# Kernel optimization log

Hardware: AMD Instinct MI355X
Metric: run time of the kernel (lower is better)

The kernel has to match this reference:

```python
import jax, jax.numpy as jnp
import numpy as np

B_, C_, H_, W_ = 8, 128, 64, 64
OUT_ = 128
D_MODEL = C_ // 4        # 32, per-chunk channels fed to Mamba
D_STATE = 16
D_CONV = 4
D_INNER = 2 * D_MODEL    # expand=2 -> 64
DT_RANK = max(1, -(-D_MODEL // 16))  # ceil(32/16)=2
SE_RED = 2


def _ln(x, g, b):
    m = x.mean(-1, keepdims=True)
    v = jnp.var(x, axis=-1, keepdims=True)
    return (x - m) / jnp.sqrt(v + 1e-5) * g + b


def _mamba(u, in_W, conv_W, conv_b, xproj_W, dt_W, dt_b, A_log, D_p, out_W):
    # u: (B, L, d_model)
    Bsz, L, _ = u.shape
    xz = u @ in_W.T                                   # (B,L,2*d_inner)
    x, z = jnp.split(xz, 2, axis=-1)
    # causal depthwise conv1d along L
    xc = jnp.swapaxes(x, 1, 2)                        # (B,d_inner,L)
    xc = jax.lax.conv_general_dilated(
        xc, conv_W, (1,), [(D_CONV - 1, 0)],
        feature_group_count=D_INNER,
        dimension_numbers=('NCH', 'OIH', 'NCH'))
    x = jax.nn.silu(jnp.swapaxes(xc + conv_b[None, :, None], 1, 2))
    x_dbl = x @ xproj_W.T                             # (B,L,dt_rank+2*d_state)
    dt, Bm, Cm = jnp.split(x_dbl, [DT_RANK, DT_RANK + D_STATE], axis=-1)
    dt = jax.nn.softplus(dt @ dt_W.T + dt_b)          # (B,L,d_inner)
    A = -jnp.exp(A_log)                               # (d_inner,d_state)
    dA = jnp.exp(dt[..., None] * A)                   # (B,L,d_inner,d_state)
    dBu = dt[..., None] * Bm[:, :, None, :] * x[..., None]

    def step(h, inp):
        dA_t, dBu_t, C_t = inp
        h = dA_t * h + dBu_t                          # (B,d_inner,d_state)
        return h, jnp.einsum('bds,bs->bd', h, C_t)

    h0 = jnp.zeros((Bsz, D_INNER, D_STATE), dtype=x.dtype)
    _, ys = jax.lax.scan(step, h0, (jnp.swapaxes(dA, 0, 1), jnp.swapaxes(dBu, 0, 1), jnp.swapaxes(Cm, 0, 1)))
    y = jnp.swapaxes(ys, 0, 1) + x * D_p
    y = y * jax.nn.silu(z)
    return y @ out_W.T


def _branch(xi, skip_scale, se_W1, se_W2, mp):
    M1 = _mamba(xi, *mp)                              # (B,L,c)
    M2 = skip_scale * xi
    # SE: adaptive avg-pool over spatial == mean over tokens; cat over channels
    y = jnp.concatenate([M1, M2], axis=-1).mean(axis=1)   # (B,2c)
    y = jax.nn.sigmoid(jax.nn.relu(y @ se_W1.T) @ se_W2.T)
    g1, g2 = jnp.split(y, 2, axis=-1)
    return g1[:, None, :] * M1 + g2[:, None, :] * M2


def _pvm(x, norm_g, norm_b, proj_W, proj_b, skip_scale, se_W1, se_W2,
         in_W, conv_W, conv_b, xproj_W, dt_W, dt_b, A_log, D_p, out_W):
    B, C, H, W = x.shape
    L = H * W
    xf = jnp.swapaxes(x.reshape(B, C, L), 1, 2)       # (B,L,C)
    xn = _ln(xf, norm_g, norm_b)
    mp = (in_W, conv_W, conv_b, xproj_W, dt_W, dt_b, A_log, D_p, out_W)
    outs = [_branch(c, skip_scale, se_W1, se_W2, mp) for c in jnp.split(xn, 4, axis=2)]
    xm = jnp.concatenate(outs, axis=2)                # (B,L,C)
    xm = _ln(xm, norm_g, norm_b)
    xm = xm @ proj_W.T + proj_b                       # (B,L,out)
    return jnp.swapaxes(xm, 1, 2).reshape(B, proj_W.shape[0], H, W)


def setup_inputs():
    key = jax.random.key(0)
    ks = jax.random.split(key, 10)
    p = {}
    p['x'] = jax.random.normal(ks[0], (B_, C_, H_, W_), jnp.float32)
    p['norm_g'] = jnp.ones((C_,), jnp.float32)
    p['norm_b'] = jnp.zeros((C_,), jnp.float32)
    p['proj_W'] = jax.random.normal(ks[1], (OUT_, C_), jnp.float32) * 0.05
    p['proj_b'] = jnp.zeros((OUT_,), jnp.float32)
    p['skip_scale'] = jnp.ones((1,), jnp.float32)
    p['se_W1'] = jax.random.normal(ks[2], (SE_RED, 2 * D_MODEL), jnp.float32) * 0.1
    p['se_W2'] = jax.random.normal(ks[3], (2 * D_MODEL, SE_RED), jnp.float32) * 0.1
    p['in_W'] = jax.random.normal(ks[4], (2 * D_INNER, D_MODEL), jnp.float32) * 0.1
    p['conv_W'] = jax.random.normal(ks[5], (D_INNER, 1, D_CONV), jnp.float32) * 0.2
    p['conv_b'] = jnp.zeros((D_INNER,), jnp.float32)
    p['xproj_W'] = jax.random.normal(ks[6], (DT_RANK + 2 * D_STATE, D_INNER), jnp.float32) * 0.1
    p['dt_W'] = jax.random.normal(ks[7], (D_INNER, DT_RANK), jnp.float32) * 0.1
    p['dt_b'] = jnp.full((D_INNER,), -4.6, jnp.float32)  # softplus(-4.6) ~ 0.01 init dt
    p['A_log'] = jnp.log(jnp.broadcast_to(jnp.arange(1.0, D_STATE + 1.0, dtype=jnp.float32), (D_INNER, D_STATE)))
    p['D_p'] = jnp.ones((D_INNER,), jnp.float32)
    p['out_W'] = jax.random.normal(ks[8], (D_MODEL, D_INNER), jnp.float32) * 0.1
    return p


def reference(x, norm_g, norm_b, proj_W, proj_b, skip_scale, se_W1, se_W2,
              in_W, conv_W, conv_b, xproj_W, dt_W, dt_b, A_log, D_p, out_W):
    return _pvm(x, norm_g, norm_b, proj_W, proj_b, skip_scale, se_W1, se_W2,
                in_W, conv_W, conv_b, xproj_W, dt_W, dt_b, A_log, D_p, out_W)
```

## Files before the change

### kernel.cpp

```cpp
#include <hip/hip_runtime.h>
#include <math.h>

typedef _Float16 h16;

#define DEV static __device__ __forceinline__

constexpr int B_ = 8, C_ = 128, L_ = 4096, OUT_ = 128;
constexpr int NCH = 4, DM = 32, DS = 16, DI = 64;
constexpr int NI = 32;
constexpr int NSEG = 128;
constexpr int SL = L_ / NSEG;

DEV float sigmoidf_(float x) { return 1.f / (1.f + __expf(-x)); }
DEV float siluf_(float x) { return x * sigmoidf_(x); }
DEV float softplusf_(float x) { return (x > 20.f) ? x : __logf(1.f + __expf(x)); }

template <int CTRL>
DEV float dpp_add_(float x) {
  int v = __builtin_amdgcn_update_dpp(0, __float_as_int(x), CTRL, 0xf, 0xf, false);
  return x + __int_as_float(v);
}

typedef __attribute__((ext_vector_type(8))) _Float16 f16x8;
typedef __attribute__((ext_vector_type(4))) _Float16 f16x4;
typedef __attribute__((ext_vector_type(4))) float f32x4;

DEV void powladder_(float E, float* out) {
  float E2 = E * E;
  float E4 = E2 * E2;
  float E8 = E4 * E4;
  float E3 = E2 * E;
  out[0] = E;       out[1] = E2;      out[2] = E3;      out[3] = E4;
  out[4] = E4 * E;  out[5] = E4 * E2; out[6] = E4 * E3; out[7] = E8;
  out[8] = E8 * E;  out[9] = E8 * E2; out[10] = E8 * E3; out[11] = E8 * E4;
  out[12] = E8 * out[4]; out[13] = E8 * out[5]; out[14] = E8 * out[6];
  out[15] = E8 * E8;
}

DEV void powladder8_(float E, float* out) {
  float E2 = E * E, E3 = E2 * E, E4 = E2 * E2;
  out[0] = E; out[1] = E2; out[2] = E3; out[3] = E4;
  out[4] = E4 * E; out[5] = E4 * E2; out[6] = E4 * E3; out[7] = E4 * E4;
}

__global__ __launch_bounds__(256) void k0_wcvt(const float* __restrict__ in_W,
                                               const float* __restrict__ xproj_W,
                                               h16* __restrict__ WH) {
  int tid = blockIdx.x * 256 + threadIdx.x;
  if (tid < 4096) {
    WH[tid] = (h16)in_W[tid];
  } else {
    int j = tid - 4096;
    int r = j >> 6;
    WH[tid] = (r < 34) ? (h16)xproj_W[j - (r - (r < 34 ? 0 : 0)) * 0 + (r * 64 + (j & 63)) - j + j] : (h16)0.f;
    WH[tid] = (r < 34) ? (h16)xproj_W[r * 64 + (j & 63)] : (h16)0.f;
  }
}

__global__ __launch_bounds__(256) void k1_ln(const float* __restrict__ x,
                                             const float* __restrict__ gn,
                                             const float* __restrict__ bn,
                                             float* __restrict__ XN,
                                             h16* __restrict__ XNH,
                                             float* __restrict__ SUMXN) {
  int bid = blockIdx.x;
  int b = bid >> 6, tile = bid & 63;
  int t0 = tile * 64;
  int tid = threadIdx.x;
  __shared__ float xT[128][65];
  __shared__ float gnS[128], bnS[128];
  __shared__ float red[256];
  if (tid < 128) { gnS[tid] = gn[tid]; bnS[tid] = bn[tid]; }
  for (int k = tid; k < 8192; k += 256) {
    int c = k >> 6, tt = k & 63;
    xT[c][tt] = x[((size_t)(b * C_ + c)) * L_ + t0 + tt];
  }
  __syncthreads();
  {
    int tok = tid >> 2, q = tid & 3;
    float s = 0.f, qq = 0.f;
#pragma unroll
    for (int j = 0; j < 32; ++j) {
      float v = xT[q + 4 * j][tok];
      s += v; qq += v * v;
    }
    s = dpp_add_<0xB1>(s); qq = dpp_add_<0xB1>(qq);
    s = dpp_add_<0x4E>(s); qq = dpp_add_<0x4E>(qq);
    float m = s * (1.f / 128.f);
    float var = qq * (1.f / 128.f) - m * m;
    float rs = rsqrtf(var + 1e-5f);
#pragma unroll
    for (int j = 0; j < 32; ++j) {
      int c = q + 4 * j;
      float v = xT[c][tok];
      xT[c][tok] = (v - m) * rs * gnS[c] + bnS[c];
    }
  }
  __syncthreads();
  float acc = 0.f;
  int cfix = tid & 127;
  for (int k = tid; k < 8192; k += 256) {
    int tt = k >> 7, c = k & 127;
    float v = xT[c][tt];
    XN[((size_t)(b * L_ + t0 + tt)) * C_ + c] = v;
    acc += v;
  }
  for (int k = tid; k < 1024; k += 256) {
    int tt = k >> 4, c8 = (k & 15) * 8;
    f16x8 hv;
#pragma unroll
    for (int j = 0; j < 8; ++j) hv[j] = (_Float16)xT[c8 + j][tt];
    *(f16x8*)&XNH[((size_t)(b * L_ + t0 + tt)) * C_ + c8] = hv;
  }
  red[tid] = acc;
  __syncthreads();
  if (tid < 128) atomicAdd(&SUMXN[b * C_ + cfix], red[tid] + red[tid + 128]);
}

__global__ __launch_bounds__(256) void k2_prep(
    const h16* __restrict__ WH, const float* __restrict__ conv_W,
    const float* __restrict__ conv_b, const float* __restrict__ dt_W,
    const float* __restrict__ dt_b, const float* __restrict__ A_log,
    const h16* __restrict__ XNH, h16* __restrict__ SX2, h16* __restrict__ SDT2,
    h16* __restrict__ SB2, h16* __restrict__ SC2, h16* __restrict__ SZ2,
    float* __restrict__ Pp, float* __restrict__ Qp) {
  int bid = blockIdx.x;
  int i = bid >> 6, tile = bid & 63;
  int b = i >> 2, ch = i & 3;
  int t0 = tile * 64;
  int tid = threadIdx.x;
  int w = __builtin_amdgcn_readfirstlane(tid >> 6);
  int lane = tid & 63;

  __shared__ __attribute__((aligned(16))) union {
    struct {
      _Float16 uH[80][40];
      _Float16 w1H[64][40];
    } s;
    float xdS[64][36];
    _Float16 zL[64][88];
  } U;
  __shared__ __attribute__((aligned(16))) _Float16 wzH[64][40];
  __shared__ __attribute__((aligned(16))) _Float16 preH[80][66];
  __shared__ __attribute__((aligned(16))) _Float16 xH[64][72];
  __shared__ __attribute__((aligned(16))) _Float16 w2H[48][72];
  __shared__ float convWS[64][4];
  __shared__ float dtWS[64][2];
  __shared__ float dtbS[64], cbS[64];

  convWS[tid >> 2][tid & 3] = conv_W[tid];
  if (tid < 128) dtWS[tid >> 1][tid & 1] = dt_W[tid];
  if (tid < 64) { dtbS[tid] = dt_b[tid]; cbS[tid] = conv_b[tid]; }
  const h16* xnh = XNH + (size_t)b * L_ * C_ + ch * DM;
  for (int k = tid; k < 320; k += 256) {
    int r = k >> 2, c8 = (k & 3) * 8;
    int tg = t0 - 3 + r;
    f16x8 v = {0, 0, 0, 0, 0, 0, 0, 0};
    if (r < 67 && tg >= 0) v = *(const f16x8*)&xnh[(size_t)tg * C_ + c8];
    *(f16x8*)&U.s.uH[r][c8] = v;
  }
  if (tid < 256) {
    int r = tid >> 2, c8 = (tid & 3) * 8;
    *(f16x8*)&U.s.w1H[r][c8] = *(const f16x8*)&WH[r * 32 + c8];
    *(f16x8*)&wzH[r][c8] = *(const f16x8*)&WH[(64 + r) * 32 + c8];
  }
  for (int k = tid; k < 384; k += 256) {
    int r = k >> 3, c8 = (k & 7) * 8;
    *(f16x8*)&w2H[r][c8] = *(const f16x8*)&WH[4096 + r * 64 + c8];
  }
  __syncthreads();

  int rsel = lane & 15, ksel = (lane >> 4) * 8;
  {
    int nt = w;
    f16x8 bf = *(const f16x8*)&U.s.w1H[nt * 16 + rsel][ksel];
    int row0q = (lane >> 4) << 2;
    int col = nt * 16 + rsel;
#pragma unroll
    for (int mt = 0; mt < 5; ++mt) {
      f16x8 af = *(const f16x8*)&U.s.uH[mt * 16 + rsel][ksel];
      f32x4 acc = {0.f, 0.f, 0.f, 0.f};
      acc = __builtin_amdgcn_mfma_f32_16x16x32_f16(af, bf, acc, 0, 0, 0);
      int row0 = mt * 16 + row0q;
#pragma unroll
      for (int r = 0; r < 4; ++r) preH[row0 + r][col] = (_Float16)acc[r];
    }
  }
  f32x4 zacc[4];
  {
    f16x8 bf = *(const f16x8*)&U.s.uH[3 + w * 16 + rsel][ksel];
#pragma unroll
    for (int mt = 0; mt < 4; ++mt) {
      f16x8 af = *(const f16x8*)&wzH[mt * 16 + rsel][ksel];
      f32x4 acc = {0.f, 0.f, 0.f, 0.f};
      zacc[mt] = __builtin_amdgcn_mfma_f32_16x16x32_f16(af, bf, acc, 0, 0, 0);
    }
  }
  __syncthreads();

  h16* SXp = SX2 + ((size_t)i * L_ + t0) * DI;
  for (int k = tid; k < 4096; k += 256) {
    int r = k >> 6, d = k & 63;
    float v = cbS[d];
#pragma unroll
    for (int j = 0; j < 4; ++j) v = fmaf(convWS[d][j], (float)preH[r + j][d], v);
    v = siluf_(v);
    xH[r][d] = (_Float16)v;
    SXp[(size_t)r * DI + d] = (h16)v;
  }
  __syncthreads();

  {
    int mt = w;
    f16x8 a0 = *(const f16x8*)&xH[mt * 16 + rsel][ksel];
    f16x8 a1 = *(const f16x8*)&xH[mt * 16 + rsel][32 + ksel];
    int row0 = mt * 16 + ((lane >> 4) << 2);
#pragma unroll
    for (int nt = 0; nt < 3; ++nt) {
      f16x8 b0 = *(const f16x8*)&w2H[nt * 16 + rsel][ksel];
      f16x8 b1 = *(const f16x8*)&w2H[nt * 16 + rsel][32 + ksel];
      f32x4 acc = {0.f, 0.f, 0.f, 0.f};
      acc = __builtin_amdgcn_mfma_f32_16x16x32_f16(a0, b0, acc, 0, 0, 0);
      acc = __builtin_amdgcn_mfma_f32_16x16x32_f16(a1, b1, acc, 0, 0, 0);
      int col = nt * 16 + rsel;
      if (col < 34) {
#pragma unroll
        for (int r = 0; r < 4; ++r) U.xdS[row0 + r][col] = acc[r];
      }
    }
  }
  __syncthreads();

  h16* dtL = (h16*)&preH[0][0];
  h16* SDTp = SDT2 + ((size_t)i * L_ + t0) * DI;
  for (int k = tid; k < 4096; k += 256) {
    int d = k & 63, r = k >> 6;
    float raw = fmaf(U.xdS[r][0], dtWS[d][0], fmaf(U.xdS[r][1], dtWS[d][1], dtbS[d]));
    float dtv = softplusf_(raw);
    dtL[r * 66 + d] = (_Float16)dtv;
    SDTp[(size_t)r * DI + d] = (h16)dtv;
  }
  h16* SBp = SB2 + ((size_t)i * L_ + t0) * DS;
  h16* SCp = SC2 + ((size_t)i * L_ + t0) * DS;
  for (int k = tid; k < 1024; k += 256) {
    int s = k & 15, r = k >> 4;
    SBp[(size_t)r * DS + s] = (h16)U.xdS[r][2 + s];
    SCp[(size_t)r * DS + s] = (h16)U.xdS[r][18 + s];
  }
  __syncthreads();

  {
    int seg = w >> 1, shalf = w & 1;
    int s0 = shalf * 8;
    float Av[16];
#pragma unroll
    for (int s = 0; s < 16; ++s) Av[s] = -__expf(A_log[lane * 16 + s]);
    float A0 = Av[0];
    bool okf = true;
#pragma unroll
    for (int s = 0; s < 16; ++s)
      okf &= fabsf(Av[s] - (float)(s + 1) * A0) <= 1e-4f * fabsf(Av[s]);
    int fastp = __all(okf ? 1 : 0);
    float h[8];
#pragma unroll
    for (int j = 0; j < 8; ++j) h[j] = 0.f;
    float sdt = 0.f;
    int rowbase = seg * SL;
    for (int t = 0; t < SL; ++t) {
      int row = rowbase + t;
      float dt = (float)dtL[row * 66 + lane];
      float xv = (float)xH[row][lane];
      float dtx = dt * xv;
      float dA[8];
      if (fastp) {
        powladder8_(__expf(A0 * dt), dA);
        if (shalf) {
          float E8 = dA[7];
#pragma unroll
          for (int j = 0; j < 8; ++j) dA[j] *= E8;
        }
      } else {
#pragma unroll
        for (int j = 0; j < 8; ++j) dA[j] = __expf(Av[s0 + j] * dt);
      }
      const float* brow = &U.xdS[row][2 + s0];
#pragma unroll
      for (int j = 0; j < 8; ++j) h[j] = fmaf(dA[j], h[j], dtx * brow[j]);
      sdt += dt;
    }
    float P[8];
    if (fastp) {
      powladder8_(__expf(A0 * sdt), P);
      if (shalf) {
        float E8 = P[7];
#pragma unroll
        for (int j = 0; j < 8; ++j) P[j] *= E8;
      }
    } else {
#pragma unroll
      for (int j = 0; j < 8; ++j) P[j] = __expf(Av[s0 + j] * sdt);
    }
    int segg = tile * 2 + seg;
    size_t base = (((size_t)i * DI + lane) * NSEG + segg) * DS + s0;
    *(float4*)(Pp + base) = *(float4*)&P[0];
    *(float4*)(Pp + base + 4) = *(float4*)&P[4];
    *(float4*)(Qp + base) = *(float4*)&h[0];
    *(float4*)(Qp + base + 4) = *(float4*)&h[4];
  }
  __syncthreads();

  {
    int tok = w * 16 + rsel;
    int zq = (lane >> 4) << 2;
#pragma unroll
    for (int mt = 0; mt < 4; ++mt) {
      f16x4 pk;
#pragma unroll
      for (int r = 0; r < 4; ++r) pk[r] = (_Float16)siluf_(zacc[mt][r]);
      *(f16x4*)&U.zL[tok][mt * 16 + zq] = pk;
    }
  }
  __syncthreads();
  h16* SZp = SZ2 + ((size_t)i * L_ + t0) * DI;
  for (int k = tid; k < 512; k += 256) {
    int r = k >> 3, dblk = (k & 7) * 8;
    f16x8 v = *(const f16x8*)&U.zL[r][dblk];
    *(f16x8*)&SZp[(size_t)r * DI + dblk] = v;
  }
}

__global__ __launch_bounds__(256) void k3b_comb(float* __restrict__ Pp,
                                                const float* __restrict__ Qp) {
  int g = blockIdx.x * 256 + threadIdx.x;
  int s = g & 15;
  int r = g >> 4;
  size_t base = (size_t)r * NSEG * DS + s;
  float H = 0.f;
  for (int seg = 0; seg < NSEG; ++seg) {
    size_t a = base + (size_t)seg * DS;
    float P = Pp[a], Q = Qp[a];
    Pp[a] = H;
    H = fmaf(P, H, Q);
  }
}

__global__ __launch_bounds__(256) void k3c_scan(
    const float* __restrict__ A_log, const h16* __restrict__ SDT2,
    const h16* __restrict__ SX2, const h16* __restrict__ SB2,
    const h16* __restrict__ SC2, const h16* __restrict__ SZ2,
    const float* __restrict__ D_p, const float* __restrict__ H0p,
    h16* __restrict__ YS2, float* __restrict__ SUMYF) {
  int bid = blockIdx.x;
  int i = bid >> 5, sg = bid & 31;
  int tid = threadIdx.x;
  int w = tid >> 6, lane = tid & 63;
  int seg = sg * 4 + w;
  int t0 = seg * SL;
  __shared__ float rowS[4][SL][36];
  {
    int tk = lane & 31, hf = lane >> 5;
    const h16* p = (hf ? SC2 : SB2) + ((size_t)i * L_ + t0 + tk) * DS;
    float4 r0 = *(const float4*)p;
    float4 r1 = *(const float4*)(p + 8);
    const h16* hp0 = (const h16*)&r0;
    const h16* hp1 = (const h16*)&r1;
#pragma unroll
    for (int s = 0; s < 8; ++s) {
      rowS[w][tk][hf * 16 + s] = (float)hp0[s];
      rowS[w][tk][hf * 16 + 8 + s] = (float)hp1[s];
    }
  }
  __syncthreads();
  float Av[16];
#pragma unroll
  for (int s = 0; s < 16; ++s) Av[s] = -__expf(A_log[lane * 16 + s]);
  float A0 = Av[0];
  bool okf = true;
#pragma unroll
  for (int s = 0; s < 16; ++s) okf &= fabsf(Av[s] - (float)(s + 1) * A0) <= 1e-4f * fabsf(Av[s]);
  int fastp = __all(okf ? 1 : 0);
  float Dp = D_p[lane];
  float h[16];
  {
    size_t base = (((size_t)i * DI + lane) * NSEG + seg) * DS;
#pragma unroll
    for (int j = 0; j < 4; ++j) *(float4*)&h[4 * j] = *(const float4*)(H0p + base + 4 * j);
  }
  const h16* pdt = SDT2 + ((size_t)i * L_ + t0) * DI + lane;
  const h16* pxx = SX2 + ((size_t)i * L_ + t0) * DI + lane;
  const h16* pzz = SZ2 + ((size_t)i * L_ + t0) * DI + lane;
  h16* pys = YS2 + ((size_t)i * L_ + t0) * DI + lane;
  float dtc = (float)pdt[0], xvc = (float)pxx[0], zvc = (float)pzz[0];
  float sum = 0.f;
  for (int t = 0; t < SL; ++t) {
    float dt = dtc, xv = xvc, zv = zvc;
    if (t < SL - 1) {
      dtc = (float)pdt[(t + 1) * DI];
      xvc = (float)pxx[(t + 1) * DI];
      zvc = (float)pzz[(t + 1) * DI];
    }
    const float* row = &rowS[w][t][0];
    float Bv[16], Cv[16];
#pragma unroll
    for (int j = 0; j < 4; ++j) {
      *(float4*)&Bv[4 * j] = *(const float4*)(row + 4 * j);
      *(float4*)&Cv[4 * j] = *(const float4*)(row + 16 + 4 * j);
    }
    float dtx = dt * xv;
    float dA[16];
    if (fastp) {
      powladder_(__expf(A0 * dt), dA);
    } else {
#pragma unroll
      for (int s = 0; s < 16; ++s) dA[s] = __expf(Av[s] * dt);
    }
    float y0 = 0.f, y1 = 0.f, y2 = 0.f, y3 = 0.f;
#pragma unroll
    for (int s = 0; s < 16; s += 4) {
      h[s] = fmaf(dA[s], h[s], dtx * Bv[s]);       y0 = fmaf(h[s], Cv[s], y0);
      h[s + 1] = fmaf(dA[s + 1], h[s + 1], dtx * Bv[s + 1]); y1 = fmaf(h[s + 1], Cv[s + 1], y1);
      h[s + 2] = fmaf(dA[s + 2], h[s + 2], dtx * Bv[s + 2]); y2 = fmaf(h[s + 2], Cv[s + 2], y2);
      h[s + 3] = fmaf(dA[s + 3], h[s + 3], dtx * Bv[s + 3]); y3 = fmaf(h[s + 3], Cv[s + 3], y3);
    }
    float y = (y0 + y1) + (y2 + y3);
    float yf = fmaf(xv, Dp, y) * zv;
    pys[(size_t)t * DI] = (h16)yf;
    sum += yf;
  }
  atomicAdd(&SUMYF[i * DI + lane], sum);
}

__global__ __launch_bounds__(64) void k4_gates(
    const float* __restrict__ out_W, const float* __restrict__ se_W1,
    const float* __restrict__ se_W2, const float* __restrict__ skip_p,
    const float* __restrict__ SUMYF, const float* __restrict__ SUMXN,
    float* __restrict__ GATES) {
  int i = blockIdx.x;
  int b = i >> 2, ch = i & 3;
  int tid = threadIdx.x;
  __shared__ float syS[64], catS[64], seS[2];
  syS[tid] = SUMYF[i * DI + tid];
  __syncthreads();
  float invL = 1.f / (float)L_;
  if (tid < 32) {
    float acc = 0.f;
#pragma unroll
    for (int dd = 0; dd < 64; ++dd) acc = fmaf(syS[dd], out_W[tid * 64 + dd], acc);
    catS[tid] = acc * invL;
  } else {
    int c = tid - 32;
    catS[tid] = skip_p[0] * SUMXN[b * C_ + ch * DM + c] * invL;
  }
  __syncthreads();
  if (tid < 2) {
    float acc = 0.f;
#pragma unroll
    for (int k = 0; k < 64; ++k) acc = fmaf(catS[k], se_W1[tid * 64 + k], acc);
    seS[tid] = fmaxf(acc, 0.f);
  }
  __syncthreads();
  float gg = fmaf(seS[0], se_W2[tid * 2 + 0], seS[1] * se_W2[tid * 2 + 1]);
  GATES[i * DI + tid] = sigmoidf_(gg);
}

__global__ __launch_bounds__(256) void k5b_combine(
    const float* __restrict__ out_W, const float* __restrict__ skip_p,
    const float* __restrict__ GATES, const h16* __restrict__ YS2,
    float* __restrict__ XN) {
  int bid = blockIdx.x;
  int i = bid >> 6, tile = bid & 63;
  int b = i >> 2, ch = i & 3;
  int t0 = tile * 64;
  int tid = threadIdx.x;
  int w = __builtin_amdgcn_readfirstlane(tid >> 6);
  int lane = tid & 63;
  __shared__ __attribute__((aligned(16))) _Float16 yH[64][72];
  __shared__ __attribute__((aligned(16))) _Float16 owH[32][72];
  __shared__ float xnS[64][37];
  __shared__ float gS[64];
  if (tid < 64) gS[tid] = GATES[i * DI + tid];
  const h16* py = YS2 + ((size_t)i * L_ + t0) * DI;
  for (int k = tid; k < 512; k += 256) {
    int tt = k >> 3, dblk = (k & 7) * 8;
    *(f16x8*)&yH[tt][dblk] = *(const f16x8*)&py[(size_t)tt * DI + dblk];
  }
  for (int k = tid; k < 2048; k += 256) owH[k >> 6][k & 63] = (_Float16)out_W[k];
  float* xn = XN + (size_t)b * L_ * C_ + ch * DM;
  for (int k = tid; k < 2048; k += 256) {
    int tt = k >> 5, o = k & 31;
    xnS[tt][o] = xn[(size_t)(t0 + tt) * C_ + o];
  }
  __syncthreads();
  int rsel = lane & 15, ksel = (lane >> 4) * 8;
  float skip = skip_p[0];
  int mt = w;
  f16x8 a0 = *(const f16x8*)&yH[mt * 16 + rsel][ksel];
  f16x8 a1 = *(const f16x8*)&yH[mt * 16 + rsel][32 + ksel];
  int row0 = mt * 16 + ((lane >> 4) << 2);
#pragma unroll
  for (int nt = 0; nt < 2; ++nt) {
    f16x8 b0 = *(const f16x8*)&owH[nt * 16 + rsel][ksel];
    f16x8 b1 = *(const f16x8*)&owH[nt * 16 + rsel][32 + ksel];
    f32x4 acc = {0.f, 0.f, 0.f, 0.f};
    acc = __builtin_amdgcn_mfma_f32_16x16x32_f16(a0, b0, acc, 0, 0, 0);
    acc = __builtin_amdgcn_mfma_f32_16x16x32_f16(a1, b1, acc, 0, 0, 0);
    int o = nt * 16 + rsel;
    float g1 = gS[o], g2s = gS[32 + o] * skip;
#pragma unroll
    for (int r = 0; r < 4; ++r) {
      int tok = row0 + r;
      xnS[tok][o] = g1 * acc[r] + g2s * xnS[tok][o];
    }
  }
  __syncthreads();
  for (int k = tid; k < 2048; k += 256) {
    int tt = k >> 5, o = k & 31;
    xn[(size_t)(t0 + tt) * C_ + o] = xnS[tt][o];
  }
}

__global__ __launch_bounds__(256) void k6_ln_proj(
    const float* __restrict__ gn, const float* __restrict__ bn,
    const float* __restrict__ proj_W, const float* __restrict__ proj_b,
    const float* __restrict__ XN, float* __restrict__ out) {
  int bid = blockIdx.x;
  int b = bid >> 6, tile = bid & 63;
  int t0 = tile * 64;
  int tid = threadIdx.x;
  int w = __builtin_amdgcn_readfirstlane(tid >> 6);
  int lane = tid & 63;
  __shared__ __attribute__((aligned(16))) union {
    float xmS[64][132];
    _Float16 projH[128][136];
  } U;
  __shared__ __attribute__((aligned(16))) _Float16 xmH[64][136];
  __shared__ float gnS[128], bnS[128];
  if (tid < 128) { gnS[tid] = gn[tid]; bnS[tid] = bn[tid]; }
  const float* xm = XN + (size_t)b * L_ * C_;
  for (int k = tid; k < 8192; k += 256) {
    int tt = k >> 7, c = k & 127;
    U.xmS[tt][c] = xm[(size_t)(t0 + tt) * C_ + c];
  }
  __syncthreads();
  {
    int tok = tid >> 2, q = tid & 3;
    float s = 0.f, qq = 0.f;
#pragma unroll
    for (int j = 0; j < 32; ++j) {
      float v = U.xmS[tok][4 * j + q];
      s += v; qq += v * v;
    }
    s = dpp_add_<0xB1>(s); qq = dpp_add_<0xB1>(qq);
    s = dpp_add_<0x4E>(s); qq = dpp_add_<0x4E>(qq);
    float m = s * (1.f / 128.f);
    float var = qq * (1.f / 128.f) - m * m;
    float rs = rsqrtf(var + 1e-5f);
#pragma unroll
    for (int j = 0; j < 32; ++j) {
      int c = 4 * j + q;
      float v = U.xmS[tok][c];
      U.xmS[tok][c] = (v - m) * rs * gnS[c] + bnS[c];
    }
  }
  __syncthreads();
  for (int k = tid; k < 1024; k += 256) {
    int tt = k >> 4, cblk = (k & 15) * 8;
    float4 v0 = *(const float4*)&U.xmS[tt][cblk];
    float4 v1 = *(const float4*)&U.xmS[tt][cblk + 4];
    f16x8 hv;
    hv[0] = (_Float16)v0.x; hv[1] = (_Float16)v0.y;
    hv[2] = (_Float16)v0.z; hv[3] = (_Float16)v0.w;
    hv[4] = (_Float16)v1.x; hv[5] = (_Float16)v1.y;
    hv[6] = (_Float16)v1.z; hv[7] = (_Float16)v1.w;
    *(f16x8*)&xmH[tt][cblk] = hv;
  }
  __syncthreads();
  for (int k = tid; k < 2048; k += 256) {
    int o = k >> 4, cblk = (k & 15) * 8;
    const float* wp = proj_W + o * 128 + cblk;
    float4 v0 = *(const float4*)wp;
    float4 v1 = *(const float4*)(wp + 4);
    f16x8 hv;
    hv[0] = (_Float16)v0.x; hv[1] = (_Float16)v0.y;
    hv[2] = (_Float16)v0.z; hv[3] = (_Float16)v0.w;
    hv[4] = (_Float16)v1.x; hv[5] = (_Float16)v1.y;
    hv[6] = (_Float16)v1.z; hv[7] = (_Float16)v1.w;
    *(f16x8*)&U.projH[o][cblk] = hv;
  }
  __syncthreads();
  int rsel = lane & 15, ksel = (lane >> 4) * 8;
  int mt = w;
  f16x8 af[4];
#pragma unroll
  for (int kc = 0; kc < 4; ++kc)
    af[kc] = *(const f16x8*)&xmH[mt * 16 + rsel][kc * 32 + ksel];
  int row0 = mt * 16 + ((lane >> 4) << 2);
#pragma unroll
  for (int nt = 0; nt < 8; ++nt) {
    int o = nt * 16 + rsel;
    float pb = proj_b[o];
    f32x4 acc = {pb, pb, pb, pb};
#pragma unroll
    for (int kc = 0; kc < 4; ++kc) {
      f16x8 bf = *(const f16x8*)&U.projH[o][kc * 32 + ksel];
      acc = __builtin_amdgcn_mfma_f32_16x16x32_f16(af[kc], bf, acc, 0, 0, 0);
    }
    *(float4*)&out[((size_t)(b * OUT_ + o)) * L_ + t0 + row0] =
        make_float4(acc[0], acc[1], acc[2], acc[3]);
  }
}

extern "C" void kernel_launch(void* const* d_in, const int* in_sizes, int n_in,
                              void* d_out, int out_size, void* d_ws, size_t ws_size,
                              hipStream_t stream) {
  const float* x = (const float*)d_in[0];
  const float* norm_g = (const float*)d_in[1];
  const float* norm_b = (const float*)d_in[2];
  const float* proj_W = (const float*)d_in[3];
  const float* proj_b = (const float*)d_in[4];
  const float* skip = (const float*)d_in[5];
  const float* se_W1 = (const float*)d_in[6];
  const float* se_W2 = (const float*)d_in[7];
  const float* in_W = (const float*)d_in[8];
  const float* conv_W = (const float*)d_in[9];
  const float* conv_b = (const float*)d_in[10];
  const float* xproj_W = (const float*)d_in[11];
  const float* dt_W = (const float*)d_in[12];
  const float* dt_b = (const float*)d_in[13];
  const float* A_log = (const float*)d_in[14];
  const float* D_p = (const float*)d_in[15];
  const float* out_W = (const float*)d_in[16];
  float* out = (float*)d_out;

  float* XN = (float*)d_ws;
  float* SUMYF = XN + (size_t)B_ * L_ * C_;
  float* SUMXN = SUMYF + NI * DI;
  float* GATES = SUMXN + B_ * C_;
  float* Pp = GATES + NI * DI;
  float* Qp = Pp + (size_t)NI * DI * NSEG * DS;
  h16* YS2 = (h16*)(Qp + (size_t)NI * DI * NSEG * DS);
  h16* SX2 = YS2 + (size_t)NI * L_ * DI;
  h16* SDT2 = SX2 + (size_t)NI * L_ * DI;
  h16* SB2 = SDT2 + (size_t)NI * L_ * DI;
  h16* SC2 = SB2 + (size_t)NI * L_ * DS;
  h16* SZ2 = SC2 + (size_t)NI * L_ * DS;
  h16* XNH = SZ2 + (size_t)NI * L_ * DI;
  h16* WH = XNH + (size_t)B_ * L_ * C_;

  hipMemsetAsync(SUMYF, 0, (size_t)(NI * DI + B_ * C_) * sizeof(float), stream);
  k0_wcvt<<<28, 256, 0, stream>>>(in_W, xproj_W, WH);
  k1_ln<<<B_ * 64, 256, 0, stream>>>(x, norm_g, norm_b, XN, XNH, SUMXN);
  k2_prep<<<NI * 64, 256, 0, stream>>>(WH, conv_W, conv_b, dt_W, dt_b, A_log,
                                       XNH, SX2, SDT2, SB2, SC2, SZ2, Pp, Qp);
  k3b_comb<<<128, 256, 0, stream>>>(Pp, Qp);
  k3c_scan<<<NI * 32, 256, 0, stream>>>(A_log, SDT2, SX2, SB2, SC2, SZ2, D_p,
                                        Pp, YS2, SUMYF);
  k4_gates<<<NI, 64, 0, stream>>>(out_W, se_W1, se_W2, skip, SUMYF, SUMXN, GATES);
  k5b_combine<<<NI * 64, 256, 0, stream>>>(out_W, skip, GATES, YS2, XN);
  k6_ln_proj<<<B_ * 64, 256, 0, stream>>>(norm_g, norm_b, proj_W, proj_b, XN, out);
}
```

Before: 226.3 us.

## Fuse gated combine into LN+projection kernel and batch prefix-combine loads

Merges the gated combine kernel (out_W matmul plus SE gating) into the final LayerNorm+projection kernel. Each block now processes all four channel chunks for its token tile, so the XN round trip through global memory and one launch go away. The sequential segment-combine loop now loads eight P/Q values ahead to expose memory-level parallelism. The z-projection weights are read directly from global memory instead of being staged in LDS. In exchange, the fused kernel serialises four chunk iterations with barriers and runs fewer blocks than the separate combine kernel did.

```diff
diff --git a/kernel.cpp b/kernel.cpp
--- a/kernel.cpp
+++ b/kernel.cpp
@@ -49,10 +49,9 @@
   int tid = blockIdx.x * 256 + threadIdx.x;
   if (tid < 4096) {
     WH[tid] = (h16)in_W[tid];
-  } else {
+  } else if (tid < 4096 + 48 * 64) {
     int j = tid - 4096;
     int r = j >> 6;
-    WH[tid] = (r < 34) ? (h16)xproj_W[j - (r - (r < 34 ? 0 : 0)) * 0 + (r * 64 + (j & 63)) - j + j] : (h16)0.f;
     WH[tid] = (r < 34) ? (h16)xproj_W[r * 64 + (j & 63)] : (h16)0.f;
   }
 }
@@ -140,7 +139,6 @@
     float xdS[64][36];
     _Float16 zL[64][88];
   } U;
-  __shared__ __attribute__((aligned(16))) _Float16 wzH[64][40];
   __shared__ __attribute__((aligned(16))) _Float16 preH[80][66];
   __shared__ __attribute__((aligned(16))) _Float16 xH[64][72];
   __shared__ __attribute__((aligned(16))) _Float16 w2H[48][72];
@@ -159,10 +157,9 @@
     if (r < 67 && tg >= 0) v = *(const f16x8*)&xnh[(size_t)tg * C_ + c8];
     *(f16x8*)&U.s.uH[r][c8] = v;
   }
-  if (tid < 256) {
+  {
     int r = tid >> 2, c8 = (tid & 3) * 8;
     *(f16x8*)&U.s.w1H[r][c8] = *(const f16x8*)&WH[r * 32 + c8];
-    *(f16x8*)&wzH[r][c8] = *(const f16x8*)&WH[(64 + r) * 32 + c8];
   }
   for (int k = tid; k < 384; k += 256) {
     int r = k >> 3, c8 = (k & 7) * 8;
@@ -191,7 +188,7 @@
     f16x8 bf = *(const f16x8*)&U.s.uH[3 + w * 16 + rsel][ksel];
 #pragma unroll
     for (int mt = 0; mt < 4; ++mt) {
-      f16x8 af = *(const f16x8*)&wzH[mt * 16 + rsel][ksel];
+      f16x8 af = *(const f16x8*)&WH[(size_t)(64 + mt * 16 + rsel) * 32 + ksel];
       f32x4 acc = {0.f, 0.f, 0.f, 0.f};
       zacc[mt] = __builtin_amdgcn_mfma_f32_16x16x32_f16(af, bf, acc, 0, 0, 0);
     }
@@ -336,11 +333,20 @@
   int r = g >> 4;
   size_t base = (size_t)r * NSEG * DS + s;
   float H = 0.f;
-  for (int seg = 0; seg < NSEG; ++seg) {
-    size_t a = base + (size_t)seg * DS;
-    float P = Pp[a], Q = Qp[a];
-    Pp[a] = H;
-    H = fmaf(P, H, Q);
+  for (int sb = 0; sb < NSEG; sb += 8) {
+    float Pv[8], Qv[8];
+#pragma unroll
+    for (int j = 0; j < 8; ++j) {
+      size_t a = base + (size_t)(sb + j) * DS;
+      Pv[j] = Pp[a];
+      Qv[j] = Qp[a];
+    }
+#pragma unroll
+    for (int j = 0; j < 8; ++j) {
+      size_t a = base + (size_t)(sb + j) * DS;
+      Pp[a] = H;
+      H = fmaf(Pv[j], H, Qv[j]);
+    }
   }
 }
 
@@ -463,63 +469,9 @@
   GATES[i * DI + tid] = sigmoidf_(gg);
 }
 
-__global__ __launch_bounds__(256) void k5b_combine(
+__global__ __launch_bounds__(256) void k56_comb_proj(
     const float* __restrict__ out_W, const float* __restrict__ skip_p,
     const float* __restrict__ GATES, const h16* __restrict__ YS2,
-    float* __restrict__ XN) {
-  int bid = blockIdx.x;
-  int i = bid >> 6, tile = bid & 63;
-  int b = i >> 2, ch = i & 3;
-  int t0 = tile * 64;
-  int tid = threadIdx.x;
-  int w = __builtin_amdgcn_readfirstlane(tid >> 6);
-  int lane = tid & 63;
-  __shared__ __attribute__((aligned(16))) _Float16 yH[64][72];
-  __shared__ __attribute__((aligned(16))) _Float16 owH[32][72];
-  __shared__ float xnS[64][37];
-  __shared__ float gS[64];
-  if (tid < 64) gS[tid] = GATES[i * DI + tid];
-  const h16* py = YS2 + ((size_t)i * L_ + t0) * DI;
-  for (int k = tid; k < 512; k += 256) {
-    int tt = k >> 3, dblk = (k & 7) * 8;
-    *(f16x8*)&yH[tt][dblk] = *(const f16x8*)&py[(size_t)tt * DI + dblk];
-  }
-  for (int k = tid; k < 2048; k += 256) owH[k >> 6][k & 63] = (_Float16)out_W[k];
-  float* xn = XN + (size_t)b * L_ * C_ + ch * DM;
-  for (int k = tid; k < 2048; k += 256) {
-    int tt = k >> 5, o = k & 31;
-    xnS[tt][o] = xn[(size_t)(t0 + tt) * C_ + o];
-  }
-  __syncthreads();
-  int rsel = lane & 15, ksel = (lane >> 4) * 8;
-  float skip = skip_p[0];
-  int mt = w;
-  f16x8 a0 = *(const f16x8*)&yH[mt * 16 + rsel][ksel];
-  f16x8 a1 = *(const f16x8*)&yH[mt * 16 + rsel][32 + ksel];
-  int row0 = mt * 16 + ((lane >> 4) << 2);
-#pragma unroll
-  for (int nt = 0; nt < 2; ++nt) {
-    f16x8 b0 = *(const f16x8*)&owH[nt * 16 + rsel][ksel];
-    f16x8 b1 = *(const f16x8*)&owH[nt * 16 + rsel][32 + ksel];
-    f32x4 acc = {0.f, 0.f, 0.f, 0.f};
-    acc = __builtin_amdgcn_mfma_f32_16x16x32_f16(a0, b0, acc, 0, 0, 0);
-    acc = __builtin_amdgcn_mfma_f32_16x16x32_f16(a1, b1, acc, 0, 0, 0);
-    int o = nt * 16 + rsel;
-    float g1 = gS[o], g2s = gS[32 + o] * skip;
-#pragma unroll
-    for (int r = 0; r < 4; ++r) {
-      int tok = row0 + r;
-      xnS[tok][o] = g1 * acc[r] + g2s * xnS[tok][o];
-    }
-  }
-  __syncthreads();
-  for (int k = tid; k < 2048; k += 256) {
-    int tt = k >> 5, o = k & 31;
-    xn[(size_t)(t0 + tt) * C_ + o] = xnS[tt][o];
-  }
-}
-
-__global__ __launch_bounds__(256) void k6_ln_proj(
     const float* __restrict__ gn, const float* __restrict__ bn,
     const float* __restrict__ proj_W, const float* __restrict__ proj_b,
     const float* __restrict__ XN, float* __restrict__ out) {
@@ -533,15 +485,56 @@
     float xmS[64][132];
     _Float16 projH[128][136];
   } U;
-  __shared__ __attribute__((aligned(16))) _Float16 xmH[64][136];
+  __shared__ __attribute__((aligned(16))) union {
+    struct {
+      _Float16 yH[64][72];
+      _Float16 owH[32][72];
+    } pre;
+    _Float16 xmH[64][136];
+  } V;
+  __shared__ float gAll[4][64];
   __shared__ float gnS[128], bnS[128];
+
   if (tid < 128) { gnS[tid] = gn[tid]; bnS[tid] = bn[tid]; }
   const float* xm = XN + (size_t)b * L_ * C_;
   for (int k = tid; k < 8192; k += 256) {
     int tt = k >> 7, c = k & 127;
     U.xmS[tt][c] = xm[(size_t)(t0 + tt) * C_ + c];
   }
-  __syncthreads();
+  if (tid < 256) gAll[tid >> 6][tid & 63] = GATES[(b * 4 + (tid >> 6)) * DI + (tid & 63)];
+  for (int k = tid; k < 2048; k += 256) V.pre.owH[k >> 6][k & 63] = (_Float16)out_W[k];
+
+  int rsel = lane & 15, ksel = (lane >> 4) * 8;
+  float skip = skip_p[0];
+  for (int ch = 0; ch < 4; ++ch) {
+    const h16* py = YS2 + ((size_t)(b * 4 + ch) * L_ + t0) * DI;
+    for (int k = tid; k < 512; k += 256) {
+      int tt = k >> 3, dblk = (k & 7) * 8;
+      *(f16x8*)&V.pre.yH[tt][dblk] = *(const f16x8*)&py[(size_t)tt * DI + dblk];
+    }
+    __syncthreads();
+    f16x8 a0 = *(const f16x8*)&V.pre.yH[w * 16 + rsel][ksel];
+    f16x8 a1 = *(const f16x8*)&V.pre.yH[w * 16 + rsel][32 + ksel];
+    int row0 = w * 16 + ((lane >> 4) << 2);
+#pragma unroll
+    for (int nt = 0; nt < 2; ++nt) {
+      f16x8 b0 = *(const f16x8*)&V.pre.owH[nt * 16 + rsel][ksel];
+      f16x8 b1 = *(const f16x8*)&V.pre.owH[nt * 16 + rsel][32 + ksel];
+      f32x4 acc = {0.f, 0.f, 0.f, 0.f};
+      acc = __builtin_amdgcn_mfma_f32_16x16x32_f16(a0, b0, acc, 0, 0, 0);
+      acc = __builtin_amdgcn_mfma_f32_16x16x32_f16(a1, b1, acc, 0, 0, 0);
+      int o = nt * 16 + rsel;
+      float g1 = gAll[ch][o], g2s = gAll[ch][32 + o] * skip;
+      int cc = ch * 32 + o;
+#pragma unroll
+      for (int r = 0; r < 4; ++r) {
+        int tok = row0 + r;
+        U.xmS[tok][cc] = g1 * acc[r] + g2s * U.xmS[tok][cc];
+      }
+    }
+    __syncthreads();
+  }
+
   {
     int tok = tid >> 2, q = tid & 3;
     float s = 0.f, qq = 0.f;
@@ -572,7 +565,7 @@
     hv[2] = (_Float16)v0.z; hv[3] = (_Float16)v0.w;
     hv[4] = (_Float16)v1.x; hv[5] = (_Float16)v1.y;
     hv[6] = (_Float16)v1.z; hv[7] = (_Float16)v1.w;
-    *(f16x8*)&xmH[tt][cblk] = hv;
+    *(f16x8*)&V.xmH[tt][cblk] = hv;
   }
   __syncthreads();
   for (int k = tid; k < 2048; k += 256) {
@@ -588,13 +581,11 @@
     *(f16x8*)&U.projH[o][cblk] = hv;
   }
   __syncthreads();
-  int rsel = lane & 15, ksel = (lane >> 4) * 8;
-  int mt = w;
   f16x8 af[4];
 #pragma unroll
   for (int kc = 0; kc < 4; ++kc)
-    af[kc] = *(const f16x8*)&xmH[mt * 16 + rsel][kc * 32 + ksel];
-  int row0 = mt * 16 + ((lane >> 4) << 2);
+    af[kc] = *(const f16x8*)&V.xmH[w * 16 + rsel][kc * 32 + ksel];
+  int row0 = w * 16 + ((lane >> 4) << 2);
 #pragma unroll
   for (int nt = 0; nt < 8; ++nt) {
     int o = nt * 16 + rsel;
@@ -656,6 +647,6 @@
   k3c_scan<<<NI * 32, 256, 0, stream>>>(A_log, SDT2, SX2, SB2, SC2, SZ2, D_p,
                                         Pp, YS2, SUMYF);
   k4_gates<<<NI, 64, 0, stream>>>(out_W, se_W1, se_W2, skip, SUMYF, SUMXN, GATES);
-  k5b_combine<<<NI * 64, 256, 0, stream>>>(out_W, skip, GATES, YS2, XN);
-  k6_ln_proj<<<B_ * 64, 256, 0, stream>>>(norm_g, norm_b, proj_W, proj_b, XN, out);
-}
+  k56_comb_proj<<<B_ * 64, 256, 0, stream>>>(out_W, skip, GATES, YS2, norm_g,
+                                             norm_b, proj_W, proj_b, XN, out);
+}
```

New measurement: 214.1 us. 5.4% less time.
